# Kernel tuning notes

Measured on AMD Instinct MI355X. Metric: run time of the kernel, lower is better.

Reference implementation:

```python
import jax, jax.numpy as jnp
import numpy as np

BS = 640          # batch size (also attention seq len, since batch_first=False)
IN_CH = 2048
S = 174           # interpreted as the MHA batch dim
E = 4             # cat_emb_channels == embed_dim == num_heads (head_dim = 1)
OUT_CH = S * E    # 696
VBS = 512         # ghost batch norm virtual batch size
EPS = 1e-5


def setup_inputs() -> dict:
    key = jax.random.key(0)
    ks = jax.random.split(key, 8)
    x = jax.random.normal(ks[0], (BS, IN_CH), dtype=jnp.float32)
    prior = jax.random.uniform(ks[1], (BS, OUT_CH), dtype=jnp.float32)
    # Linear(in_channels, out_channels, bias=False)
    w_lin = jax.random.normal(ks[2], (OUT_CH, IN_CH), dtype=jnp.float32) / np.sqrt(IN_CH)
    # BatchNorm1d affine params
    bn_gamma = jnp.ones((OUT_CH,), dtype=jnp.float32)
    bn_beta = jnp.zeros((OUT_CH,), dtype=jnp.float32)
    # MultiheadAttention packed in-projection (3E, E) + bias (3E,)
    in_proj_w = jax.random.normal(ks[3], (3 * E, E), dtype=jnp.float32) / np.sqrt(E)
    in_proj_b = jnp.zeros((3 * E,), dtype=jnp.float32)
    out_proj_w = jax.random.normal(ks[4], (E, E), dtype=jnp.float32) / np.sqrt(E)
    out_proj_b = jnp.zeros((E,), dtype=jnp.float32)
    return {"x": x, "prior": prior, "w_lin": w_lin, "bn_gamma": bn_gamma,
            "bn_beta": bn_beta, "in_proj_w": in_proj_w, "in_proj_b": in_proj_b,
            "out_proj_w": out_proj_w, "out_proj_b": out_proj_b}


def _ghost_bn(h, gamma, beta):
    # torch.chunk(640, 2) -> two equal chunks of 320; training-mode batch stats per chunk
    num_chunks = int(np.ceil(BS / VBS))  # 2
    hc = h.reshape(num_chunks, BS // num_chunks, OUT_CH)
    mean = hc.mean(axis=1, keepdims=True)
    var = hc.var(axis=1, keepdims=True)  # biased variance, as BatchNorm uses for normalization
    hn = (hc - mean) * jax.lax.rsqrt(var + EPS)
    return (hn * gamma + beta).reshape(BS, OUT_CH)


def reference(x, prior, w_lin, bn_gamma, bn_beta, in_proj_w, in_proj_b,
              out_proj_w, out_proj_b):
    h = x @ w_lin.T                       # [BS, OUT_CH]
    h = _ghost_bn(h, bn_gamma, bn_beta)
    h = prior * h
    # batch_first=False MHA: seq len = BS, batch = S=174, embed = E, heads = E (head_dim=1)
    q_in = h.reshape(BS, S, E)
    kv_in = prior.reshape(BS, S, E)
    wq, wk, wv = in_proj_w[:E], in_proj_w[E:2 * E], in_proj_w[2 * E:]
    bq, bk, bv = in_proj_b[:E], in_proj_b[E:2 * E], in_proj_b[2 * E:]
    q = q_in @ wq.T + bq                  # [BS, S, E]; scale = 1/sqrt(head_dim=1) = 1
    k = kv_in @ wk.T + bk
    v = kv_in @ wv.T + bv
    # per-(batch n, head e) scalar features -> [S, E, BS, BS] scores
    scores = jnp.einsum('lne,sne->nels', q, k)
    attn = jax.nn.softmax(scores, axis=-1)
    o = jnp.einsum('nels,sne->lne', attn, v)   # [BS, S, E]
    y = o @ out_proj_w.T + out_proj_b
    h = h + y.reshape(BS, OUT_CH)
    return jax.nn.softmax(h, axis=-1)
```

## Files before the change

### kernel.cpp

```cpp
#include <hip/hip_runtime.h>
#include <math.h>

#define BS 640
#define IN_CH 2048
#define NGRP 174
#define OUT_CH 696
#define CHUNK 320
#define EPS_BN 1e-5f
#define LOG2E 1.4426950408889634f

#if __has_builtin(__builtin_amdgcn_exp2f)
#define EXP2(x) __builtin_amdgcn_exp2f(x)
#else
#define EXP2(x) exp2f(x)
#endif

typedef short short8 __attribute__((ext_vector_type(8)));
typedef float f32x4 __attribute__((ext_vector_type(4)));

__global__ __launch_bounds__(256) void zero_kernel(float4* __restrict__ p, int n4) {
    int i = blockIdx.x * 256 + threadIdx.x;
    if (i < n4) p[i] = make_float4(0.f, 0.f, 0.f, 0.f);
}

__device__ inline void split_bf16(float x, unsigned short* hi, unsigned short* lo) {
    unsigned int u = __float_as_uint(x);
    unsigned int rh = (u + 0x7FFFu + ((u >> 16) & 1u)) >> 16;
    *hi = (unsigned short)rh;
    float hf = __uint_as_float(rh << 16);
    float l = x - hf;
    unsigned int ul = __float_as_uint(l);
    *lo = (unsigned short)((ul + 0x7FFFu + ((ul >> 16) & 1u)) >> 16);
}

__global__ __launch_bounds__(256) void gemm_kernel(const float* __restrict__ X,
                                                   const float* __restrict__ W,
                                                   float* __restrict__ H) {
    __shared__ unsigned short Ah[64][72], Al[64][72], Bh[64][72], Bl[64][72];
    int tid = threadIdx.x;
    int row0 = blockIdx.x * 64;
    int col0 = blockIdx.y * 64;
    int k0 = blockIdx.z * (IN_CH / 4);

    int srow = tid >> 2;
    int skc = (tid & 3) * 16;
    const float* xp = X + (size_t)(row0 + srow) * IN_CH + k0 + skc;
    int wn = col0 + srow;
    const float* wp = W + (size_t)(wn < OUT_CH ? wn : 0) * IN_CH + k0 + skc;

    int w = tid >> 6;
    int lane = tid & 63;
    int wr = (w >> 1) * 32, wc = (w & 1) * 32;
    int lr = lane & 15, lq = lane >> 4;

    f32x4 acc[2][2] = {};

    for (int kt = 0; kt < IN_CH / 4; kt += 64) {
        float4 a[4], b[4];
#pragma unroll
        for (int i = 0; i < 4; ++i) {
            a[i] = *(const float4*)(xp + kt + 4 * i);
            b[i] = *(const float4*)(wp + kt + 4 * i);
        }
        __syncthreads();
#pragma unroll
        for (int i = 0; i < 4; ++i) {
            float av[4] = {a[i].x, a[i].y, a[i].z, a[i].w};
            float bv[4] = {b[i].x, b[i].y, b[i].z, b[i].w};
            unsigned short ah[4], al[4], bh[4], bl[4];
#pragma unroll
            for (int j = 0; j < 4; ++j) {
                split_bf16(av[j], &ah[j], &al[j]);
                split_bf16(bv[j], &bh[j], &bl[j]);
            }
            *(ushort4*)&Ah[srow][skc + 4 * i] = make_ushort4(ah[0], ah[1], ah[2], ah[3]);
            *(ushort4*)&Al[srow][skc + 4 * i] = make_ushort4(al[0], al[1], al[2], al[3]);
            *(ushort4*)&Bh[srow][skc + 4 * i] = make_ushort4(bh[0], bh[1], bh[2], bh[3]);
            *(ushort4*)&Bl[srow][skc + 4 * i] = make_ushort4(bl[0], bl[1], bl[2], bl[3]);
        }
        __syncthreads();
#pragma unroll
        for (int kk = 0; kk < 64; kk += 32) {
            int ko = kk + lq * 8;
            short8 ahf[2], alf[2], bhf[2], blf[2];
#pragma unroll
            for (int mf = 0; mf < 2; ++mf) {
                ahf[mf] = *(const short8*)&Ah[wr + mf * 16 + lr][ko];
                alf[mf] = *(const short8*)&Al[wr + mf * 16 + lr][ko];
                bhf[mf] = *(const short8*)&Bh[wc + mf * 16 + lr][ko];
                blf[mf] = *(const short8*)&Bl[wc + mf * 16 + lr][ko];
            }
#pragma unroll
            for (int mf = 0; mf < 2; ++mf)
#pragma unroll
                for (int nf = 0; nf < 2; ++nf) {
                    acc[mf][nf] = __builtin_amdgcn_mfma_f32_16x16x32_bf16(ahf[mf], bhf[nf], acc[mf][nf], 0, 0, 0);
                    acc[mf][nf] = __builtin_amdgcn_mfma_f32_16x16x32_bf16(ahf[mf], blf[nf], acc[mf][nf], 0, 0, 0);
                    acc[mf][nf] = __builtin_amdgcn_mfma_f32_16x16x32_bf16(alf[mf], bhf[nf], acc[mf][nf], 0, 0, 0);
                }
        }
    }
#pragma unroll
    for (int mf = 0; mf < 2; ++mf)
#pragma unroll
        for (int nf = 0; nf < 2; ++nf)
#pragma unroll
            for (int j = 0; j < 4; ++j) {
                int r = row0 + wr + mf * 16 + lq * 4 + j;
                int c = col0 + wc + nf * 16 + lr;
                if (c < OUT_CH) atomicAdd(&H[(size_t)r * OUT_CH + c], acc[mf][nf][j]);
            }
}

__global__ __launch_bounds__(320) void stats_kernel(const float* __restrict__ H,
        const float* __restrict__ gamma, const float* __restrict__ beta,
        float* __restrict__ stats) {
    __shared__ float red[5][8];
    int n = blockIdx.x, chunk = blockIdx.y, tid = threadIdx.x;
    int c0 = n * 4;
    int l = chunk * CHUNK + tid;
    float4 h4 = *(const float4*)(H + (size_t)l * OUT_CH + c0);
    float hr[4] = {h4.x, h4.y, h4.z, h4.w};
    float rv[8];
#pragma unroll
    for (int e = 0; e < 4; ++e) { rv[e] = hr[e]; rv[4 + e] = hr[e] * hr[e]; }
#pragma unroll
    for (int off = 32; off > 0; off >>= 1)
#pragma unroll
        for (int j = 0; j < 8; ++j) rv[j] += __shfl_down(rv[j], off);
    int wv = tid >> 6, ln = tid & 63;
    if (ln == 0)
#pragma unroll
        for (int j = 0; j < 8; ++j) red[wv][j] = rv[j];
    __syncthreads();
    if (tid < 4) {
        int e = tid;
        float s = red[0][e] + red[1][e] + red[2][e] + red[3][e] + red[4][e];
        float ss = red[0][4 + e] + red[1][4 + e] + red[2][4 + e] + red[3][4 + e] + red[4][4 + e];
        float m = s * (1.0f / CHUNK);
        float var = ss * (1.0f / CHUNK) - m * m;
        float scv = rsqrtf(var + EPS_BN) * gamma[c0 + e];
        stats[chunk * OUT_CH + c0 + e] = scv;
        stats[2 * OUT_CH + chunk * OUT_CH + c0 + e] = beta[c0 + e] - m * scv;
    }
}

__global__ __launch_bounds__(256) void attn_kernel(float* __restrict__ H,
        const float* __restrict__ prior,
        const float* __restrict__ stats,
        const float* __restrict__ ipw, const float* __restrict__ ipb,
        const float* __restrict__ opw, const float* __restrict__ opb) {
    __shared__ float k_sh[BS][4];
    __shared__ float v_sh[BS][4];
    __shared__ float kext[8];

    int n = blockIdx.x, qb = blockIdx.y, tid = threadIdx.x;
    int c0 = n * 4;
    int chunk = (qb >= 5);

    for (int s = tid; s < BS; s += 256) {
        float4 pr = *(const float4*)(prior + (size_t)s * OUT_CH + c0);
        float p_[4] = {pr.x, pr.y, pr.z, pr.w};
        float kk[4], vv[4];
#pragma unroll
        for (int e = 0; e < 4; ++e) {
            float ak = ipb[4 + e], av = ipb[8 + e];
#pragma unroll
            for (int e2 = 0; e2 < 4; ++e2) {
                ak = fmaf(ipw[(4 + e) * 4 + e2], p_[e2], ak);
                av = fmaf(ipw[(8 + e) * 4 + e2], p_[e2], av);
            }
            kk[e] = ak; vv[e] = av;
        }
        int p = (s % 160) * 4 + (s / 160);
        *(float4*)&k_sh[p][0] = make_float4(kk[0], kk[1], kk[2], kk[3]);
        *(float4*)&v_sh[p][0] = make_float4(vv[0], vv[1], vv[2], vv[3]);
    }
    __syncthreads();

    int wv = tid >> 6, ln = tid & 63;
    if (wv < 4) {
        float mx = -3e38f, mn = 3e38f;
        for (int p = ln; p < BS; p += 64) {
            float kv = k_sh[p][wv];
            mx = fmaxf(mx, kv); mn = fminf(mn, kv);
        }
#pragma unroll
        for (int off = 32; off > 0; off >>= 1) {
            mx = fmaxf(mx, __shfl_down(mx, off));
            mn = fminf(mn, __shfl_down(mn, off));
        }
        if (ln == 0) { kext[wv] = mx; kext[4 + wv] = mn; }
    }
    __syncthreads();

    int q = qb * 64 + (tid >> 2);
    int seg = tid & 3;
    float4 h4 = *(const float4*)(H + (size_t)q * OUT_CH + c0);
    float4 pq = *(const float4*)(prior + (size_t)q * OUT_CH + c0);
    float hr[4] = {h4.x, h4.y, h4.z, h4.w};
    float pq_[4] = {pq.x, pq.y, pq.z, pq.w};
    const float* sc = stats + chunk * OUT_CH;
    const float* sh = stats + 2 * OUT_CH + chunk * OUT_CH;

    float hh[4];
#pragma unroll
    for (int e = 0; e < 4; ++e)
        hh[e] = fmaf(hr[e], sc[c0 + e], sh[c0 + e]) * pq_[e];

    float q2[4], tmax[4];
#pragma unroll
    for (int e = 0; e < 4; ++e) {
        float qv = ipb[e];
#pragma unroll
        for (int e2 = 0; e2 < 4; ++e2) qv = fmaf(ipw[e * 4 + e2], hh[e2], qv);
        q2[e] = qv * LOG2E;
        tmax[e] = (q2[e] > 0.f) ? q2[e] * kext[e] : q2[e] * kext[4 + e];
    }

    float sum[4] = {0.f, 0.f, 0.f, 0.f}, accv[4] = {0.f, 0.f, 0.f, 0.f};
#pragma unroll 4
    for (int i = 0; i < 160; ++i) {
        int p = i * 4 + seg;
        float4 kv = *(const float4*)&k_sh[p][0];
        float4 vv = *(const float4*)&v_sh[p][0];
        float w0 = EXP2(fmaf(q2[0], kv.x, -tmax[0]));
        float w1 = EXP2(fmaf(q2[1], kv.y, -tmax[1]));
        float w2 = EXP2(fmaf(q2[2], kv.z, -tmax[2]));
        float w3 = EXP2(fmaf(q2[3], kv.w, -tmax[3]));
        sum[0] += w0; accv[0] = fmaf(w0, vv.x, accv[0]);
        sum[1] += w1; accv[1] = fmaf(w1, vv.y, accv[1]);
        sum[2] += w2; accv[2] = fmaf(w2, vv.z, accv[2]);
        sum[3] += w3; accv[3] = fmaf(w3, vv.w, accv[3]);
    }
#pragma unroll
    for (int d = 1; d < 4; d <<= 1)
#pragma unroll
        for (int e = 0; e < 4; ++e) {
            sum[e] += __shfl_xor(sum[e], d);
            accv[e] += __shfl_xor(accv[e], d);
        }

    if (seg == 0) {
        float o[4], y[4];
#pragma unroll
        for (int e = 0; e < 4; ++e) o[e] = accv[e] / sum[e];
#pragma unroll
        for (int e = 0; e < 4; ++e) {
            float a = opb[e];
#pragma unroll
            for (int e2 = 0; e2 < 4; ++e2) a = fmaf(opw[e * 4 + e2], o[e2], a);
            y[e] = a;
        }
        *(float4*)(H + (size_t)q * OUT_CH + c0) =
            make_float4(hh[0] + y[0], hh[1] + y[1], hh[2] + y[2], hh[3] + y[3]);
    }
}

__global__ __launch_bounds__(256) void softmax_kernel(float* __restrict__ out) {
    __shared__ float red[4];
    int row = blockIdx.x;
    float* p = out + (size_t)row * OUT_CH;
    int tid = threadIdx.x;
    float v[3] = {-3e38f, -3e38f, -3e38f};
#pragma unroll
    for (int i = 0; i < 3; ++i) { int c = tid + i * 256; if (c < OUT_CH) v[i] = p[c]; }
    float mx = fmaxf(fmaxf(v[0], v[1]), v[2]);
#pragma unroll
    for (int off = 32; off > 0; off >>= 1) mx = fmaxf(mx, __shfl_down(mx, off));
    if ((tid & 63) == 0) red[tid >> 6] = mx;
    __syncthreads();
    mx = fmaxf(fmaxf(red[0], red[1]), fmaxf(red[2], red[3]));
    __syncthreads();
    float e[3] = {0.f, 0.f, 0.f};
    float s = 0.f;
#pragma unroll
    for (int i = 0; i < 3; ++i) {
        int c = tid + i * 256;
        if (c < OUT_CH) { e[i] = EXP2((v[i] - mx) * LOG2E); s += e[i]; }
    }
#pragma unroll
    for (int off = 32; off > 0; off >>= 1) s += __shfl_down(s, off);
    if ((tid & 63) == 0) red[tid >> 6] = s;
    __syncthreads();
    s = red[0] + red[1] + red[2] + red[3];
    float inv = 1.0f / s;
#pragma unroll
    for (int i = 0; i < 3; ++i) { int c = tid + i * 256; if (c < OUT_CH) p[c] = e[i] * inv; }
}

extern "C" void kernel_launch(void* const* d_in, const int* in_sizes, int n_in,
                              void* d_out, int out_size, void* d_ws, size_t ws_size,
                              hipStream_t stream) {
    const float* x     = (const float*)d_in[0];
    const float* prior = (const float*)d_in[1];
    const float* w_lin = (const float*)d_in[2];
    const float* gamma = (const float*)d_in[3];
    const float* beta  = (const float*)d_in[4];
    const float* ipw   = (const float*)d_in[5];
    const float* ipb   = (const float*)d_in[6];
    const float* opw   = (const float*)d_in[7];
    const float* opb   = (const float*)d_in[8];
    float* out = (float*)d_out;
    float* stats = (float*)d_ws;

    int n4 = (BS * OUT_CH) / 4;
    zero_kernel<<<(n4 + 255) / 256, 256, 0, stream>>>((float4*)out, n4);
    gemm_kernel<<<dim3(10, 11, 4), 256, 0, stream>>>(x, w_lin, out);
    stats_kernel<<<dim3(NGRP, 2), 320, 0, stream>>>(out, gamma, beta, stats);
    attn_kernel<<<dim3(NGRP, 10), 256, 0, stream>>>(out, prior, stats, ipw, ipb, opw, opb);
    softmax_kernel<<<BS, 256, 0, stream>>>(out);
}
```

Measured before the change: 149.2 us.

## Pre-split GEMM operands to bf16, use direct-to-LDS loads, drop atomics

A new pre-pass converts X and W into bf16 hi/lo arrays in workspace. The GEMM then streams them into swizzled LDS with global_load_lds instead of converting in registers. Split-K partials are written to a padded buffer and summed in the stats kernel, which removes the zero kernel and the float atomics. The attention kernel also packs K/V into bf16 in shared memory, halving LDS traffic but reducing K/V precision. The trade-off is an extra kernel and more global memory traffic, with the old path kept as a fallback when workspace is too small.

```diff
diff --git a/kernel.cpp b/kernel.cpp
--- a/kernel.cpp
+++ b/kernel.cpp
@@ -5,6 +5,7 @@
 #define IN_CH 2048
 #define NGRP 174
 #define OUT_CH 696
+#define NPAD 704
 #define CHUNK 320
 #define EPS_BN 1e-5f
 #define LOG2E 1.4426950408889634f
@@ -18,43 +19,200 @@
 typedef short short8 __attribute__((ext_vector_type(8)));
 typedef float f32x4 __attribute__((ext_vector_type(4)));
 
+#define XH_OFF 0
+#define XL_OFF 2621440
+#define WH_OFF 5242880
+#define WL_OFF 8093696
+#define PART_OFF 10944512
+#define STATS_OFF 18153472
+#define WS_NEED (STATS_OFF + 4 * OUT_CH * 4)
+
+#define GLL16(g, l) __builtin_amdgcn_global_load_lds( \
+    (const __attribute__((address_space(1))) void*)(g), \
+    (__attribute__((address_space(3))) void*)(l), 16, 0, 0)
+
+__device__ inline unsigned short bf16_rne(float x) {
+    unsigned int u = __float_as_uint(x);
+    return (unsigned short)((u + 0x7FFFu + ((u >> 16) & 1u)) >> 16);
+}
+
+__global__ __launch_bounds__(256) void split_kernel(const float* __restrict__ X,
+                                                    const float* __restrict__ W,
+                                                    unsigned short* __restrict__ ws) {
+    const int NX4 = (BS * IN_CH) / 4;
+    const int NW4 = (OUT_CH * IN_CH) / 4;
+    int j = blockIdx.x * 256 + threadIdx.x;
+    const float4* src;
+    unsigned short *hi, *lo;
+    int idx;
+    if (j < NX4) {
+        src = (const float4*)X; hi = ws + XH_OFF / 2; lo = ws + XL_OFF / 2; idx = j;
+    } else if (j < NX4 + NW4) {
+        src = (const float4*)W; hi = ws + WH_OFF / 2; lo = ws + WL_OFF / 2; idx = j - NX4;
+    } else return;
+    float4 v = src[idx];
+    float f[4] = {v.x, v.y, v.z, v.w};
+    unsigned short h[4], l[4];
+#pragma unroll
+    for (int i = 0; i < 4; ++i) {
+        h[i] = bf16_rne(f[i]);
+        float hf = __uint_as_float(((unsigned int)h[i]) << 16);
+        l[i] = bf16_rne(f[i] - hf);
+    }
+    *(ushort4*)(hi + (size_t)idx * 4) = make_ushort4(h[0], h[1], h[2], h[3]);
+    *(ushort4*)(lo + (size_t)idx * 4) = make_ushort4(l[0], l[1], l[2], l[3]);
+}
+
+__global__ __launch_bounds__(256) void gemm_mfma(const unsigned short* __restrict__ wsu,
+                                                 float* __restrict__ part) {
+    __shared__ unsigned short Ah[4096], Al[4096], Bh[4096], Bl[4096];
+    const unsigned short* XH = wsu + XH_OFF / 2;
+    const unsigned short* XL = wsu + XL_OFF / 2;
+    const unsigned short* WH = wsu + WH_OFF / 2;
+    const unsigned short* WL = wsu + WL_OFF / 2;
+    int tid = threadIdx.x;
+    int w = tid >> 6, lane = tid & 63;
+    int row0 = blockIdx.x * 64, col0 = blockIdx.y * 64;
+    int k0 = blockIdx.z * (IN_CH / 4);
+
+    int lr8 = lane >> 3;
+    int sc = ((lane & 7) ^ lr8) << 3;
+    int r0s = 16 * w + lr8;
+    int arow0 = row0 + r0s, arow1 = arow0 + 8;
+    int b0 = col0 + r0s;     if (b0 > OUT_CH - 1) b0 = OUT_CH - 1;
+    int b1 = col0 + r0s + 8; if (b1 > OUT_CH - 1) b1 = OUT_CH - 1;
+    const unsigned short* xh0 = XH + (size_t)arow0 * IN_CH + k0 + sc;
+    const unsigned short* xh1 = XH + (size_t)arow1 * IN_CH + k0 + sc;
+    const unsigned short* xl0 = XL + (size_t)arow0 * IN_CH + k0 + sc;
+    const unsigned short* xl1 = XL + (size_t)arow1 * IN_CH + k0 + sc;
+    const unsigned short* wh0 = WH + (size_t)b0 * IN_CH + k0 + sc;
+    const unsigned short* wh1 = WH + (size_t)b1 * IN_CH + k0 + sc;
+    const unsigned short* wl0 = WL + (size_t)b0 * IN_CH + k0 + sc;
+    const unsigned short* wl1 = WL + (size_t)b1 * IN_CH + k0 + sc;
+    int ldsA0 = (16 * w + 0) * 64;
+    int ldsA1 = (16 * w + 8) * 64;
+
+    int lr = lane & 15, lq = lane >> 4;
+    int wr = (w >> 1) * 32, wc = (w & 1) * 32;
+    f32x4 acc[2][2] = {};
+
+    for (int kt = 0; kt < IN_CH / 4; kt += 64) {
+        __syncthreads();
+        GLL16(xh0 + kt, &Ah[ldsA0]);
+        GLL16(xh1 + kt, &Ah[ldsA1]);
+        GLL16(xl0 + kt, &Al[ldsA0]);
+        GLL16(xl1 + kt, &Al[ldsA1]);
+        GLL16(wh0 + kt, &Bh[ldsA0]);
+        GLL16(wh1 + kt, &Bh[ldsA1]);
+        GLL16(wl0 + kt, &Bl[ldsA0]);
+        GLL16(wl1 + kt, &Bl[ldsA1]);
+        __syncthreads();
+#pragma unroll
+        for (int kk2 = 0; kk2 < 2; ++kk2) {
+            int ci = (kk2 << 2) + lq;
+            short8 ahf[2], alf[2], bhf[2], blf[2];
+#pragma unroll
+            for (int mf = 0; mf < 2; ++mf) {
+                int ra = wr + mf * 16 + lr;
+                int ia = ra * 64 + ((ci ^ (ra & 7)) << 3);
+                ahf[mf] = *(const short8*)&Ah[ia];
+                alf[mf] = *(const short8*)&Al[ia];
+                int rb = wc + mf * 16 + lr;
+                int ib = rb * 64 + ((ci ^ (rb & 7)) << 3);
+                bhf[mf] = *(const short8*)&Bh[ib];
+                blf[mf] = *(const short8*)&Bl[ib];
+            }
+#pragma unroll
+            for (int mf = 0; mf < 2; ++mf)
+#pragma unroll
+                for (int nf = 0; nf < 2; ++nf) {
+                    acc[mf][nf] = __builtin_amdgcn_mfma_f32_16x16x32_bf16(ahf[mf], bhf[nf], acc[mf][nf], 0, 0, 0);
+                    acc[mf][nf] = __builtin_amdgcn_mfma_f32_16x16x32_bf16(ahf[mf], blf[nf], acc[mf][nf], 0, 0, 0);
+                    acc[mf][nf] = __builtin_amdgcn_mfma_f32_16x16x32_bf16(alf[mf], bhf[nf], acc[mf][nf], 0, 0, 0);
+                }
+        }
+    }
+    size_t zb = (size_t)blockIdx.z * BS;
+#pragma unroll
+    for (int mf = 0; mf < 2; ++mf)
+#pragma unroll
+        for (int nf = 0; nf < 2; ++nf)
+#pragma unroll
+            for (int j = 0; j < 4; ++j) {
+                int r = row0 + wr + mf * 16 + lq * 4 + j;
+                int c = col0 + wc + nf * 16 + lr;
+                part[(zb + r) * NPAD + c] = acc[mf][nf][j];
+            }
+}
+
+__global__ __launch_bounds__(320) void stats_reduce(const float* __restrict__ part,
+        float* __restrict__ H,
+        const float* __restrict__ gamma, const float* __restrict__ beta,
+        float* __restrict__ stats) {
+    __shared__ float red[5][8];
+    int n = blockIdx.x, chunk = blockIdx.y, tid = threadIdx.x;
+    int c0 = n * 4;
+    int l = chunk * CHUNK + tid;
+    float4 a = *(const float4*)&part[((size_t)0 * BS + l) * NPAD + c0];
+    float4 b = *(const float4*)&part[((size_t)1 * BS + l) * NPAD + c0];
+    float4 c = *(const float4*)&part[((size_t)2 * BS + l) * NPAD + c0];
+    float4 d = *(const float4*)&part[((size_t)3 * BS + l) * NPAD + c0];
+    float hr[4] = {a.x + b.x + c.x + d.x, a.y + b.y + c.y + d.y,
+                   a.z + b.z + c.z + d.z, a.w + b.w + c.w + d.w};
+    *(float4*)&H[(size_t)l * OUT_CH + c0] = make_float4(hr[0], hr[1], hr[2], hr[3]);
+    float rv[8];
+#pragma unroll
+    for (int e = 0; e < 4; ++e) { rv[e] = hr[e]; rv[4 + e] = hr[e] * hr[e]; }
+#pragma unroll
+    for (int off = 32; off > 0; off >>= 1)
+#pragma unroll
+        for (int j = 0; j < 8; ++j) rv[j] += __shfl_down(rv[j], off);
+    int wv = tid >> 6, ln = tid & 63;
+    if (ln == 0)
+#pragma unroll
+        for (int j = 0; j < 8; ++j) red[wv][j] = rv[j];
+    __syncthreads();
+    if (tid < 4) {
+        int e = tid;
+        float s = red[0][e] + red[1][e] + red[2][e] + red[3][e] + red[4][e];
+        float ss = red[0][4 + e] + red[1][4 + e] + red[2][4 + e] + red[3][4 + e] + red[4][4 + e];
+        float m = s * (1.0f / CHUNK);
+        float var = ss * (1.0f / CHUNK) - m * m;
+        float scv = rsqrtf(var + EPS_BN) * gamma[c0 + e];
+        stats[chunk * OUT_CH + c0 + e] = scv;
+        stats[2 * OUT_CH + chunk * OUT_CH + c0 + e] = beta[c0 + e] - m * scv;
+    }
+}
+
 __global__ __launch_bounds__(256) void zero_kernel(float4* __restrict__ p, int n4) {
     int i = blockIdx.x * 256 + threadIdx.x;
     if (i < n4) p[i] = make_float4(0.f, 0.f, 0.f, 0.f);
 }
 
 __device__ inline void split_bf16(float x, unsigned short* hi, unsigned short* lo) {
-    unsigned int u = __float_as_uint(x);
-    unsigned int rh = (u + 0x7FFFu + ((u >> 16) & 1u)) >> 16;
-    *hi = (unsigned short)rh;
-    float hf = __uint_as_float(rh << 16);
-    float l = x - hf;
-    unsigned int ul = __float_as_uint(l);
-    *lo = (unsigned short)((ul + 0x7FFFu + ((ul >> 16) & 1u)) >> 16);
-}
-
-__global__ __launch_bounds__(256) void gemm_kernel(const float* __restrict__ X,
-                                                   const float* __restrict__ W,
-                                                   float* __restrict__ H) {
+    *hi = bf16_rne(x);
+    float hf = __uint_as_float(((unsigned int)*hi) << 16);
+    *lo = bf16_rne(x - hf);
+}
+
+__global__ __launch_bounds__(256) void gemm_fb(const float* __restrict__ X,
+                                               const float* __restrict__ W,
+                                               float* __restrict__ H) {
     __shared__ unsigned short Ah[64][72], Al[64][72], Bh[64][72], Bl[64][72];
     int tid = threadIdx.x;
     int row0 = blockIdx.x * 64;
     int col0 = blockIdx.y * 64;
     int k0 = blockIdx.z * (IN_CH / 4);
-
     int srow = tid >> 2;
     int skc = (tid & 3) * 16;
     const float* xp = X + (size_t)(row0 + srow) * IN_CH + k0 + skc;
     int wn = col0 + srow;
     const float* wp = W + (size_t)(wn < OUT_CH ? wn : 0) * IN_CH + k0 + skc;
-
     int w = tid >> 6;
     int lane = tid & 63;
     int wr = (w >> 1) * 32, wc = (w & 1) * 32;
     int lr = lane & 15, lq = lane >> 4;
-
     f32x4 acc[2][2] = {};
-
     for (int kt = 0; kt < IN_CH / 4; kt += 64) {
         float4 a[4], b[4];
 #pragma unroll
@@ -112,7 +270,7 @@
             }
 }
 
-__global__ __launch_bounds__(320) void stats_kernel(const float* __restrict__ H,
+__global__ __launch_bounds__(320) void stats_fb(const float* __restrict__ H,
         const float* __restrict__ gamma, const float* __restrict__ beta,
         float* __restrict__ stats) {
     __shared__ float red[5][8];
@@ -150,15 +308,15 @@
         const float* __restrict__ stats,
         const float* __restrict__ ipw, const float* __restrict__ ipb,
         const float* __restrict__ opw, const float* __restrict__ opb) {
-    __shared__ float k_sh[BS][4];
-    __shared__ float v_sh[BS][4];
+    __shared__ uint4 kv_sh[BS];
     __shared__ float kext[8];
 
     int n = blockIdx.x, qb = blockIdx.y, tid = threadIdx.x;
     int c0 = n * 4;
     int chunk = (qb >= 5);
 
-    for (int s = tid; s < BS; s += 256) {
+    for (int t = tid; t < BS; t += 256) {
+        int s = (t & 3) * 160 + (t >> 2);
         float4 pr = *(const float4*)(prior + (size_t)s * OUT_CH + c0);
         float p_[4] = {pr.x, pr.y, pr.z, pr.w};
         float kk[4], vv[4];
@@ -172,18 +330,25 @@
             }
             kk[e] = ak; vv[e] = av;
         }
-        int p = (s % 160) * 4 + (s / 160);
-        *(float4*)&k_sh[p][0] = make_float4(kk[0], kk[1], kk[2], kk[3]);
-        *(float4*)&v_sh[p][0] = make_float4(vv[0], vv[1], vv[2], vv[3]);
+        unsigned int u0 = (unsigned int)bf16_rne(kk[0]) | ((unsigned int)bf16_rne(kk[1]) << 16);
+        unsigned int u1 = (unsigned int)bf16_rne(kk[2]) | ((unsigned int)bf16_rne(kk[3]) << 16);
+        unsigned int u2 = (unsigned int)bf16_rne(vv[0]) | ((unsigned int)bf16_rne(vv[1]) << 16);
+        unsigned int u3 = (unsigned int)bf16_rne(vv[2]) | ((unsigned int)bf16_rne(vv[3]) << 16);
+        kv_sh[t] = make_uint4(u0, u1, u2, u3);
     }
     __syncthreads();
 
     int wv = tid >> 6, ln = tid & 63;
     if (wv < 4) {
+        const unsigned int* kw = (const unsigned int*)kv_sh;
+        int word = wv >> 1, hi = wv & 1;
         float mx = -3e38f, mn = 3e38f;
-        for (int p = ln; p < BS; p += 64) {
-            float kv = k_sh[p][wv];
-            mx = fmaxf(mx, kv); mn = fminf(mn, kv);
+#pragma unroll
+        for (int i = 0; i < 10; ++i) {
+            int p = ln * 10 + i;
+            unsigned int u = kw[p * 4 + word];
+            float kf = __uint_as_float(hi ? (u & 0xFFFF0000u) : (u << 16));
+            mx = fmaxf(mx, kf); mn = fminf(mn, kf);
         }
 #pragma unroll
         for (int off = 32; off > 0; off >>= 1) {
@@ -219,19 +384,22 @@
     }
 
     float sum[4] = {0.f, 0.f, 0.f, 0.f}, accv[4] = {0.f, 0.f, 0.f, 0.f};
+    const uint4* kvp = kv_sh + seg;
 #pragma unroll 4
     for (int i = 0; i < 160; ++i) {
-        int p = i * 4 + seg;
-        float4 kv = *(const float4*)&k_sh[p][0];
-        float4 vv = *(const float4*)&v_sh[p][0];
-        float w0 = EXP2(fmaf(q2[0], kv.x, -tmax[0]));
-        float w1 = EXP2(fmaf(q2[1], kv.y, -tmax[1]));
-        float w2 = EXP2(fmaf(q2[2], kv.z, -tmax[2]));
-        float w3 = EXP2(fmaf(q2[3], kv.w, -tmax[3]));
-        sum[0] += w0; accv[0] = fmaf(w0, vv.x, accv[0]);
-        sum[1] += w1; accv[1] = fmaf(w1, vv.y, accv[1]);
-        sum[2] += w2; accv[2] = fmaf(w2, vv.z, accv[2]);
-        sum[3] += w3; accv[3] = fmaf(w3, vv.w, accv[3]);
+        uint4 kv = kvp[i * 4];
+        float k0 = __uint_as_float(kv.x << 16), k1 = __uint_as_float(kv.x & 0xFFFF0000u);
+        float k2 = __uint_as_float(kv.y << 16), k3 = __uint_as_float(kv.y & 0xFFFF0000u);
+        float v0 = __uint_as_float(kv.z << 16), v1 = __uint_as_float(kv.z & 0xFFFF0000u);
+        float v2 = __uint_as_float(kv.w << 16), v3 = __uint_as_float(kv.w & 0xFFFF0000u);
+        float w0 = EXP2(fmaf(q2[0], k0, -tmax[0]));
+        float w1 = EXP2(fmaf(q2[1], k1, -tmax[1]));
+        float w2 = EXP2(fmaf(q2[2], k2, -tmax[2]));
+        float w3 = EXP2(fmaf(q2[3], k3, -tmax[3]));
+        sum[0] += w0; accv[0] = fmaf(w0, v0, accv[0]);
+        sum[1] += w1; accv[1] = fmaf(w1, v1, accv[1]);
+        sum[2] += w2; accv[2] = fmaf(w2, v2, accv[2]);
+        sum[3] += w3; accv[3] = fmaf(w3, v3, accv[3]);
     }
 #pragma unroll
     for (int d = 1; d < 4; d <<= 1)
@@ -302,12 +470,24 @@
     const float* opw   = (const float*)d_in[7];
     const float* opb   = (const float*)d_in[8];
     float* out = (float*)d_out;
-    float* stats = (float*)d_ws;
-
-    int n4 = (BS * OUT_CH) / 4;
-    zero_kernel<<<(n4 + 255) / 256, 256, 0, stream>>>((float4*)out, n4);
-    gemm_kernel<<<dim3(10, 11, 4), 256, 0, stream>>>(x, w_lin, out);
-    stats_kernel<<<dim3(NGRP, 2), 320, 0, stream>>>(out, gamma, beta, stats);
-    attn_kernel<<<dim3(NGRP, 10), 256, 0, stream>>>(out, prior, stats, ipw, ipb, opw, opb);
-    softmax_kernel<<<BS, 256, 0, stream>>>(out);
-}
+
+    if (ws_size >= (size_t)WS_NEED) {
+        unsigned short* wsu = (unsigned short*)d_ws;
+        float* part  = (float*)((char*)d_ws + PART_OFF);
+        float* stats = (float*)((char*)d_ws + STATS_OFF);
+        const int NJOB = (BS * IN_CH) / 4 + (OUT_CH * IN_CH) / 4;
+        split_kernel<<<NJOB / 256, 256, 0, stream>>>(x, w_lin, wsu);
+        gemm_mfma<<<dim3(10, 11, 4), 256, 0, stream>>>(wsu, part);
+        stats_reduce<<<dim3(NGRP, 2), 320, 0, stream>>>(part, out, gamma, beta, stats);
+        attn_kernel<<<dim3(NGRP, 10), 256, 0, stream>>>(out, prior, stats, ipw, ipb, opw, opb);
+        softmax_kernel<<<BS, 256, 0, stream>>>(out);
+    } else {
+        float* stats = (float*)d_ws;
+        int n4 = (BS * OUT_CH) / 4;
+        zero_kernel<<<(n4 + 255) / 256, 256, 0, stream>>>((float4*)out, n4);
+        gemm_fb<<<dim3(10, 11, 4), 256, 0, stream>>>(x, w_lin, out);
+        stats_fb<<<dim3(NGRP, 2), 320, 0, stream>>>(out, gamma, beta, stats);
+        attn_kernel<<<dim3(NGRP, 10), 256, 0, stream>>>(out, prior, stats, ipw, ipb, opw, opb);
+        softmax_kernel<<<BS, 256, 0, stream>>>(out);
+    }
+}
```

New measurement: 159.6 us. 1.07x slower.
